# Kernel tuning notes

Hardware: AMD Instinct MI355X
Metric: run time of the kernel (lower is better)

Reference implementation:

```python
import jax, jax.numpy as jnp
import numpy as np


def _cdist(x, y):
    # Euclidean (p=2) pairwise distances, matching torch.cdist.
    # x: [B, N, D], y: [B, M, D] -> [B, N, M]
    xx = jnp.sum(x * x, axis=-1)                      # [B, N]
    yy = jnp.sum(y * y, axis=-1)                      # [B, M]
    zz = jnp.einsum('bnd,bmd->bnm', x, y)             # [B, N, M]
    d2 = xx[:, :, None] + yy[:, None, :] - 2.0 * zz
    return jnp.sqrt(jnp.maximum(d2, 0.0))


def setup_inputs() -> dict:
    key = jax.random.key(0)
    k1, k2 = jax.random.split(key)
    gts = jax.random.normal(k1, (4, 8192, 3), dtype=jnp.float32)
    preds = jax.random.normal(k2, (4, 8192, 3), dtype=jnp.float32)
    return {"gts": gts, "preds": preds}


def reference(gts, preds):
    P = _cdist(gts, preds)                 # [B, N, M]
    loss_1 = jnp.sum(jnp.min(P, axis=1), axis=1)  # min over gts points, sum over preds
    loss_2 = jnp.sum(jnp.min(P, axis=2), axis=1)  # min over preds points, sum over gts
    return loss_1 + loss_2                 # [B]
```

## Files before the change

### kernel.cpp

```cpp
#include <hip/hip_runtime.h>
#include <math.h>

#define BB 4
#define NPTS 8192
#define THREADS 512
#define NQ_TOTAL (2 * BB * NPTS)
#define QBLK 512
#define QPWV 64
#define HALFN 4096
#define CHUNK 2048
#define NCHUNK (HALFN / CHUNK)
#define NFRAG (CHUNK / 32)
#define GLDS_PER_WAVE (CHUNK / 8 / 64)
#define FBLK 256

typedef __attribute__((ext_vector_type(8)))  short bf16x8;
typedef __attribute__((ext_vector_type(16))) float f32x16;


__device__ __forceinline__ unsigned short f2bf(float f) {
    unsigned u = __float_as_uint(f);
    u += 0x7FFF + ((u >> 16) & 1);
    return (unsigned short)(u >> 16);
}
__device__ __forceinline__ float bf2f(unsigned short h) {
    return __uint_as_float(((unsigned)h) << 16);
}

__global__ __launch_bounds__(256) void pack_kernel(
    const float* __restrict__ gts, const float* __restrict__ preds,
    uint4* __restrict__ refpack, uint4* __restrict__ qpack,
    unsigned* __restrict__ minpart, float* __restrict__ out) {
    int idx = blockIdx.x * 256 + threadIdx.x;
    if (idx < BB) out[idx] = 0.0f;
    if (idx >= NQ_TOTAL) return;
    minpart[idx] = 0x7F7FFFFFu;
    int set  = idx / (BB * NPTS);
    int pidx = idx - set * (BB * NPTS);
    const float* src = set ? preds : gts;
    unsigned short hx = f2bf(src[pidx * 3 + 0]);
    unsigned short hy = f2bf(src[pidx * 3 + 1]);
    unsigned short hz = f2bf(src[pidx * 3 + 2]);
    float fx = bf2f(hx), fy = bf2f(hy), fz = bf2f(hz);
    float rr = fmaf(fx, fx, fmaf(fy, fy, fz * fz));
    unsigned short hrr = f2bf(rr);
    unsigned short hlo = f2bf(rr - bf2f(hrr));
    const unsigned short ONE = 0x3F80;

    uint4 rv;
    rv.x = (unsigned)hx  | ((unsigned)hy  << 16);
    rv.y = (unsigned)hz  | ((unsigned)hrr << 16);
    rv.z = (unsigned)hlo | ((unsigned)ONE << 16);
    rv.w = (unsigned)ONE;
    refpack[idx] = rv;

    unsigned short nx = f2bf(-2.0f * fx);
    unsigned short ny = f2bf(-2.0f * fy);
    unsigned short nz = f2bf(-2.0f * fz);
    uint4 qv;
    qv.x = (unsigned)nx  | ((unsigned)ny  << 16);
    qv.y = (unsigned)nz  | ((unsigned)ONE << 16);
    qv.z = (unsigned)ONE | ((unsigned)hrr << 16);
    qv.w = (unsigned)hlo;
    qpack[idx] = qv;
}

#define FOLD8(P, X0, X1, X2, X3)                                   \
    X0 = fminf(fminf((P)[0],  (P)[1]),  X0);                       \
    X1 = fminf(fminf((P)[2],  (P)[3]),  X1);                       \
    X2 = fminf(fminf((P)[4],  (P)[5]),  X2);                       \
    X3 = fminf(fminf((P)[6],  (P)[7]),  X3);                       \
    X0 = fminf(fminf((P)[8],  (P)[9]),  X0);                       \
    X1 = fminf(fminf((P)[10], (P)[11]), X1);                       \
    X2 = fminf(fminf((P)[12], (P)[13]), X2);                       \
    X3 = fminf(fminf((P)[14], (P)[15]), X3);

#define STEP2(AQ, FN, DO_LOAD)                                              \
    {                                                                       \
        f32x16 dn0 = __builtin_amdgcn_mfma_f32_32x32x16_bf16(AQ, bq0, zc, 0, 0, 0); \
        f32x16 dn1 = __builtin_amdgcn_mfma_f32_32x32x16_bf16(AQ, bq1, zc, 0, 0, 0); \
        if (DO_LOAD) AQ = sp[(FN) * 32 + l31];                              \
        FOLD8(pp0, c0, c1, c2, c3);                                         \
        FOLD8(pp1, c4, c5, c6, c7);                                         \
        pp0 = pc0; pc0 = dn0;                                               \
        pp1 = pc1; pc1 = dn1;                                               \
    }

#define STAGE(BUF, CBASE)                                                   \
    _Pragma("unroll")                                                       \
    for (int i = 0; i < GLDS_PER_WAVE; ++i)                                 \
        __builtin_amdgcn_global_load_lds(                                   \
            (const unsigned*)(rgl + (CBASE) + wid * 256 + i * 64 + lane),   \
            (unsigned*)&sref[BUF][wid * 256 + i * 64], 16, 0, 0);

__global__ __launch_bounds__(THREADS, 2) void chamfer_kernel(
    const uint4* __restrict__ refpack, const uint4* __restrict__ qpack,
    unsigned* __restrict__ minpart) {
    __shared__ uint4 sref[2][CHUNK];

    int tid  = threadIdx.x;
    int blk  = blockIdx.x;
    int half = blk >> 7;
    int dir  = (blk >> 6) & 1;
    int b    = (blk >> 4) & 3;
    int qg   = blk & 15;
    int rset = dir;
    int qset = dir ^ 1;
    int wid  = tid >> 6;
    int lane = tid & 63;
    int l31  = lane & 31;

    const uint4* rgl = refpack + (size_t)(rset * BB + b) * NPTS
                     + (size_t)half * HALFN;

    STAGE(0, 0);

    size_t qoff = (size_t)(qset * BB + b) * NPTS + (size_t)qg * QBLK
                + (size_t)wid * QPWV;
    bf16x8 bq0 = {0, 0, 0, 0, 0, 0, 0, 0};
    bf16x8 bq1 = {0, 0, 0, 0, 0, 0, 0, 0};
    if (lane < 32) {
        bq0 = ((const bf16x8*)qpack)[qoff + l31];
        bq1 = ((const bf16x8*)qpack)[qoff + 32 + l31];
    }
    __syncthreads();

    f32x16 zc;
    #pragma unroll
    for (int r = 0; r < 16; ++r) zc[r] = 0.0f;

    float c0 = 3.0e38f, c1 = 3.0e38f, c2 = 3.0e38f, c3 = 3.0e38f;
    float c4 = 3.0e38f, c5 = 3.0e38f, c6 = 3.0e38f, c7 = 3.0e38f;

    for (int c = 0; c < NCHUNK; ++c) {
        if (c + 1 < NCHUNK) {
            STAGE((c + 1) & 1, (c + 1) * CHUNK);
        }

        const bf16x8* sp = (const bf16x8*)sref[c & 1];

        bf16x8 a0 = sp[0 * 32 + l31];
        bf16x8 a1 = sp[1 * 32 + l31];
        bf16x8 a2 = sp[2 * 32 + l31];
        bf16x8 a3 = sp[3 * 32 + l31];
        bf16x8 a4 = sp[4 * 32 + l31];
        bf16x8 a5 = sp[5 * 32 + l31];
        bf16x8 a6 = sp[6 * 32 + l31];
        bf16x8 a7 = sp[7 * 32 + l31];

        f32x16 pp0, pc0, pp1, pc1;
        #pragma unroll
        for (int r = 0; r < 16; ++r) {
            pp0[r] = 3.0e38f; pc0[r] = 3.0e38f;
            pp1[r] = 3.0e38f; pc1[r] = 3.0e38f;
        }

        #pragma unroll
        for (int m = 0; m < NFRAG / 8; ++m) {
            const bool L = (m < NFRAG / 8 - 1);
            STEP2(a0, (m + 1) * 8 + 0, L);
            STEP2(a1, (m + 1) * 8 + 1, L);
            STEP2(a2, (m + 1) * 8 + 2, L);
            STEP2(a3, (m + 1) * 8 + 3, L);
            STEP2(a4, (m + 1) * 8 + 4, L);
            STEP2(a5, (m + 1) * 8 + 5, L);
            STEP2(a6, (m + 1) * 8 + 6, L);
            STEP2(a7, (m + 1) * 8 + 7, L);
        }
        FOLD8(pp0, c0, c1, c2, c3);
        FOLD8(pc0, c0, c1, c2, c3);
        FOLD8(pp1, c4, c5, c6, c7);
        FOLD8(pc1, c4, c5, c6, c7);

        __syncthreads();
    }

    float m0 = fminf(fminf(c0, c1), fminf(c2, c3));
    m0 = fminf(m0, __shfl_xor(m0, 32, 64));
    float m1 = fminf(fminf(c4, c5), fminf(c6, c7));
    m1 = fminf(m1, __shfl_xor(m1, 32, 64));

    size_t qid = (size_t)(dir * BB + b) * NPTS + (size_t)qg * QBLK
               + (size_t)wid * QPWV;
    if (lane < 32) {
        atomicMin(minpart + qid + l31,      __float_as_uint(fmaxf(m0, 0.0f)));
        atomicMin(minpart + qid + 32 + l31, __float_as_uint(fmaxf(m1, 0.0f)));
    }
}

__global__ __launch_bounds__(256) void merge_kernel(
    const unsigned* __restrict__ minpart, float* __restrict__ out) {
    int t  = blockIdx.x * 256 + threadIdx.x;
    uint4 v = ((const uint4*)minpart)[t];
    float d = sqrtf(__uint_as_float(v.x)) + sqrtf(__uint_as_float(v.y))
            + sqrtf(__uint_as_float(v.z)) + sqrtf(__uint_as_float(v.w));
    int b = (blockIdx.x >> 3) & 3;

    #pragma unroll
    for (int off = 32; off > 0; off >>= 1)
        d += __shfl_down(d, off, 64);

    __shared__ float wsum[4];
    int lane = threadIdx.x & 63;
    int wid  = threadIdx.x >> 6;
    if (lane == 0) wsum[wid] = d;
    __syncthreads();
    if (threadIdx.x == 0)
        atomicAdd(out + b, wsum[0] + wsum[1] + wsum[2] + wsum[3]);
}

extern "C" void kernel_launch(void* const* d_in, const int* in_sizes, int n_in,
                              void* d_out, int out_size, void* d_ws, size_t ws_size,
                              hipStream_t stream) {
    const float* gts   = (const float*)d_in[0];
    const float* preds = (const float*)d_in[1];
    float* out = (float*)d_out;

    char* ws = (char*)d_ws;
    uint4*    refpack = (uint4*)ws;
    uint4*    qpack   = (uint4*)(ws + (size_t)NQ_TOTAL * 16);
    unsigned* minpart = (unsigned*)(ws + (size_t)NQ_TOTAL * 32);

    pack_kernel<<<NQ_TOTAL / 256, 256, 0, stream>>>(
        gts, preds, refpack, qpack, minpart, out);

    chamfer_kernel<<<FBLK, THREADS, 0, stream>>>(refpack, qpack, minpart);

    merge_kernel<<<NQ_TOTAL / 4 / 256, 256, 0, stream>>>(minpart, out);
}
```

Baseline: 72.49 us.

## Split reference points into quarters across twice as many blocks, single-chunk LDS

Each block now scans a quarter of the reference set (2048 points) rather than half, so the grid doubles to 512 blocks and each block loads a single LDS chunk. That removes the double-buffered chunk loop and its barriers, and halves LDS use, which lets the launch bound allow four blocks per CU and keeps more waves resident on the GPU. The delayed fold of MFMA results (the pp/pc rotation) is dropped: results are folded right after issue, and only 4 A fragments are prefetched instead of 8. This cuts register pressure but can expose MFMA latency if the compiler does not interleave the unrolled steps. It also doubles the atomicMin traffic to the per-query minima.

```diff
diff --git a/kernel.cpp b/kernel.cpp
--- a/kernel.cpp
+++ b/kernel.cpp
@@ -7,12 +7,11 @@
 #define NQ_TOTAL (2 * BB * NPTS)
 #define QBLK 512
 #define QPWV 64
-#define HALFN 4096
+#define QUARTN 2048
 #define CHUNK 2048
-#define NCHUNK (HALFN / CHUNK)
 #define NFRAG (CHUNK / 32)
 #define GLDS_PER_WAVE (CHUNK / 8 / 64)
-#define FBLK 256
+#define FBLK 512
 
 typedef __attribute__((ext_vector_type(8)))  short bf16x8;
 typedef __attribute__((ext_vector_type(16))) float f32x16;
@@ -75,32 +74,30 @@
     X2 = fminf(fminf((P)[12], (P)[13]), X2);                       \
     X3 = fminf(fminf((P)[14], (P)[15]), X3);
 
-#define STEP2(AQ, FN, DO_LOAD)                                              \
+#define STEP(AQ, FN, DO_LOAD)                                               \
     {                                                                       \
-        f32x16 dn0 = __builtin_amdgcn_mfma_f32_32x32x16_bf16(AQ, bq0, zc, 0, 0, 0); \
-        f32x16 dn1 = __builtin_amdgcn_mfma_f32_32x32x16_bf16(AQ, bq1, zc, 0, 0, 0); \
+        f32x16 d0 = __builtin_amdgcn_mfma_f32_32x32x16_bf16(AQ, bq0, zc, 0, 0, 0); \
+        f32x16 d1 = __builtin_amdgcn_mfma_f32_32x32x16_bf16(AQ, bq1, zc, 0, 0, 0); \
         if (DO_LOAD) AQ = sp[(FN) * 32 + l31];                              \
-        FOLD8(pp0, c0, c1, c2, c3);                                         \
-        FOLD8(pp1, c4, c5, c6, c7);                                         \
-        pp0 = pc0; pc0 = dn0;                                               \
-        pp1 = pc1; pc1 = dn1;                                               \
-    }
-
-#define STAGE(BUF, CBASE)                                                   \
+        FOLD8(d0, c0, c1, c2, c3);                                          \
+        FOLD8(d1, c4, c5, c6, c7);                                          \
+    }
+
+#define STAGE()                                                             \
     _Pragma("unroll")                                                       \
     for (int i = 0; i < GLDS_PER_WAVE; ++i)                                 \
         __builtin_amdgcn_global_load_lds(                                   \
-            (const unsigned*)(rgl + (CBASE) + wid * 256 + i * 64 + lane),   \
-            (unsigned*)&sref[BUF][wid * 256 + i * 64], 16, 0, 0);
-
-__global__ __launch_bounds__(THREADS, 2) void chamfer_kernel(
+            (const unsigned*)(rgl + wid * 256 + i * 64 + lane),             \
+            (unsigned*)&sref[wid * 256 + i * 64], 16, 0, 0);
+
+__global__ __launch_bounds__(THREADS, 4) void chamfer_kernel(
     const uint4* __restrict__ refpack, const uint4* __restrict__ qpack,
     unsigned* __restrict__ minpart) {
-    __shared__ uint4 sref[2][CHUNK];
+    __shared__ uint4 sref[CHUNK];
 
     int tid  = threadIdx.x;
     int blk  = blockIdx.x;
-    int half = blk >> 7;
+    int quart= blk >> 7;
     int dir  = (blk >> 6) & 1;
     int b    = (blk >> 4) & 3;
     int qg   = blk & 15;
@@ -111,9 +108,9 @@
     int l31  = lane & 31;
 
     const uint4* rgl = refpack + (size_t)(rset * BB + b) * NPTS
-                     + (size_t)half * HALFN;
-
-    STAGE(0, 0);
+                     + (size_t)quart * QUARTN;
+
+    STAGE();
 
     size_t qoff = (size_t)(qset * BB + b) * NPTS + (size_t)qg * QBLK
                 + (size_t)wid * QPWV;
@@ -132,47 +129,20 @@
     float c0 = 3.0e38f, c1 = 3.0e38f, c2 = 3.0e38f, c3 = 3.0e38f;
     float c4 = 3.0e38f, c5 = 3.0e38f, c6 = 3.0e38f, c7 = 3.0e38f;
 
-    for (int c = 0; c < NCHUNK; ++c) {
-        if (c + 1 < NCHUNK) {
-            STAGE((c + 1) & 1, (c + 1) * CHUNK);
-        }
-
-        const bf16x8* sp = (const bf16x8*)sref[c & 1];
-
-        bf16x8 a0 = sp[0 * 32 + l31];
-        bf16x8 a1 = sp[1 * 32 + l31];
-        bf16x8 a2 = sp[2 * 32 + l31];
-        bf16x8 a3 = sp[3 * 32 + l31];
-        bf16x8 a4 = sp[4 * 32 + l31];
-        bf16x8 a5 = sp[5 * 32 + l31];
-        bf16x8 a6 = sp[6 * 32 + l31];
-        bf16x8 a7 = sp[7 * 32 + l31];
-
-        f32x16 pp0, pc0, pp1, pc1;
-        #pragma unroll
-        for (int r = 0; r < 16; ++r) {
-            pp0[r] = 3.0e38f; pc0[r] = 3.0e38f;
-            pp1[r] = 3.0e38f; pc1[r] = 3.0e38f;
-        }
-
-        #pragma unroll
-        for (int m = 0; m < NFRAG / 8; ++m) {
-            const bool L = (m < NFRAG / 8 - 1);
-            STEP2(a0, (m + 1) * 8 + 0, L);
-            STEP2(a1, (m + 1) * 8 + 1, L);
-            STEP2(a2, (m + 1) * 8 + 2, L);
-            STEP2(a3, (m + 1) * 8 + 3, L);
-            STEP2(a4, (m + 1) * 8 + 4, L);
-            STEP2(a5, (m + 1) * 8 + 5, L);
-            STEP2(a6, (m + 1) * 8 + 6, L);
-            STEP2(a7, (m + 1) * 8 + 7, L);
-        }
-        FOLD8(pp0, c0, c1, c2, c3);
-        FOLD8(pc0, c0, c1, c2, c3);
-        FOLD8(pp1, c4, c5, c6, c7);
-        FOLD8(pc1, c4, c5, c6, c7);
-
-        __syncthreads();
+    const bf16x8* sp = (const bf16x8*)sref;
+
+    bf16x8 a0 = sp[0 * 32 + l31];
+    bf16x8 a1 = sp[1 * 32 + l31];
+    bf16x8 a2 = sp[2 * 32 + l31];
+    bf16x8 a3 = sp[3 * 32 + l31];
+
+    #pragma unroll
+    for (int m = 0; m < NFRAG / 4; ++m) {
+        const bool L = (m < NFRAG / 4 - 1);
+        STEP(a0, (m + 1) * 4 + 0, L);
+        STEP(a1, (m + 1) * 4 + 1, L);
+        STEP(a2, (m + 1) * 4 + 2, L);
+        STEP(a3, (m + 1) * 4 + 3, L);
     }
 
     float m0 = fminf(fminf(c0, c1), fminf(c2, c3));
```

Result: no change. 72.44 us (-0.1%).
